# Kernel optimization log

Measured on AMD Instinct MI355X. Metric: run time of the kernel, lower is better.

Reference implementation:

```python
import jax, jax.numpy as jnp
import numpy as np

FRAMES = 8
NUM_HEADS = 12


def _build_indices_mask(N_origin):
    """Static (numpy) construction of gathered token indices and the
    multiplicative token mask (1.0 on allowed pairs, 0.8 elsewhere),
    matching token_mask + (1-token_mask)*0.8 in the torch code."""
    N = FRAMES * N_origin
    cls_idx = np.arange(0, N, N_origin)
    per_frame = [np.arange(i * N_origin + 1 + i, (i + 1) * N_origin, FRAMES)
                 for i in range(FRAMES)]
    idx = np.concatenate([cls_idx] + per_frame)
    M = idx.shape[0]
    mask = np.full((N, M), 0.8, dtype=np.float32)
    cls_len = cls_idx.shape[0]
    mask[:, :cls_len] = 1.0
    st = cls_len
    for i in range(FRAMES):
        ln = per_frame[i].shape[0]
        mask[i * N_origin:(i + 1) * N_origin, st:st + ln] = 1.0
        st += ln
    return jnp.asarray(idx), jnp.asarray(mask)


def setup_inputs() -> dict:
    key = jax.random.key(0)
    k1, k2, k3, k4 = jax.random.split(key, 4)
    C = 768
    x = jax.random.normal(k1, (64, 197, C), dtype=jnp.float32)
    qkv_w = jax.random.normal(k2, (3 * C, C), dtype=jnp.float32) * 0.02
    proj_w = jax.random.normal(k3, (C, C), dtype=jnp.float32) * 0.02
    proj_b = jax.random.normal(k4, (C,), dtype=jnp.float32) * 0.02
    return {"x": x, "qkv_w": qkv_w, "proj_w": proj_w, "proj_b": proj_b}


def reference(x, qkv_w, proj_w, proj_b):
    B0, N_origin, C = x.shape
    H = NUM_HEADS
    hd = C // H
    B = B0 // FRAMES
    N = FRAMES * N_origin
    scale = hd ** -0.5

    xg = x.reshape(B, N, C)                              # group 8 frames per video
    qkv = (xg @ qkv_w.T).reshape(B, N, 3, H, hd).transpose(2, 0, 3, 1, 4)
    q, k, v = qkv[0], qkv[1], qkv[2]                     # each [B, H, N, hd]

    idx, mask = _build_indices_mask(N_origin)            # idx [M], mask [N, M]
    k = k[:, :, idx, :]                                  # [B, H, M, hd]
    v = v[:, :, idx, :]

    attn = jnp.einsum('bhnd,bhmd->bhnm', q, k) * scale   # [B, H, N, M]
    attn = jax.nn.softmax(attn * mask, axis=-1)          # multiplicative mask, then softmax

    out = jnp.einsum('bhnm,bhmd->bhnd', attn, v)         # [B, H, N, hd]
    out = out.transpose(0, 2, 1, 3).reshape(B, N, C)
    out = out @ proj_w.T + proj_b
    return out.reshape(B0, N_origin, C)
```

## Files before the change

kernel.cpp:

```cpp
#include <hip/hip_runtime.h>
#include <stdint.h>

#define NORI   197
#define FRAMES 8
#define NTOK   1576
#define BATCH  8
#define NHEAD  12
#define CDIM   768
#define MG     204
#define TOKENS 12608

typedef _Float16 half8 __attribute__((ext_vector_type(8)));
typedef float floatx4 __attribute__((ext_vector_type(4)));

typedef const __attribute__((address_space(1))) void GPTR;
typedef __attribute__((address_space(3))) void LPTR;

__device__ __forceinline__ int gather_idx(int m) {
    if (m < 8) return m * NORI;
    int u = m - 8;
    int f, t;
    if (u < 100) { f = u / 25; t = u - f * 25; }
    else         { f = 4 + (u - 100) / 24; t = (u - 100) - (f - 4) * 24; }
    return f * NORI + 1 + f + 8 * t;
}
__device__ __forceinline__ int col_frame(int m) {
    int u = m - 8;
    return (u < 100) ? (u / 25) : (4 + (u - 100) / 24);
}

__device__ __forceinline__ int xcd_chunk(int bid, int nwg) {
    int xcd = bid & 7, j = bid >> 3;
    int q = nwg >> 3, r = nwg & 7;
    int base = (xcd < r) ? xcd * (q + 1) : r * (q + 1) + (xcd - r) * q;
    return base + j;
}

__global__ __launch_bounds__(256) void cast_all(
    const float* __restrict__ x, const float* __restrict__ qkvw,
    const float* __restrict__ projw, _Float16* __restrict__ out)
{
    const int n1 = TOKENS * CDIM / 8, n2 = 3 * CDIM * CDIM / 8, n3 = CDIM * CDIM / 8;
    const int nxb = n1 / 256;
    int bx = blockIdx.x;
    int i;
    if (bx < nxb) i = xcd_chunk(bx, nxb) * 256 + threadIdx.x;
    else          i = bx * 256 + threadIdx.x;
    if (i >= n1 + n2 + n3) return;
    const float* src; int off;
    if (i < n1)           { src = x;     off = i; }
    else if (i < n1 + n2) { src = qkvw;  off = i - n1; }
    else                  { src = projw; off = i - n1 - n2; }
    float4 a = ((const float4*)src)[2 * off];
    float4 b = ((const float4*)src)[2 * off + 1];
    half8 o = { (_Float16)a.x, (_Float16)a.y, (_Float16)a.z, (_Float16)a.w,
                (_Float16)b.x, (_Float16)b.y, (_Float16)b.z, (_Float16)b.w };
    ((half8*)out)[i] = o;
}

template <int OUT_F32>
__device__ __forceinline__ void gemm_body(
    const _Float16* __restrict__ A, const _Float16* __restrict__ W,
    const float* __restrict__ bias, void* __restrict__ Y,
    int M, int Woff, int ldY, int gather, int r0, int c0,
    _Float16* As0, _Float16* Bs0, _Float16* As1, _Float16* Bs1)
{
    const int tid = threadIdx.x;
    const int w = tid >> 6, l = tid & 63;
    const int wm = (w >> 1) * 64, wn = (w & 1) * 64;

    const _Float16* sa[2];
    const _Float16* sb[2];
    int soff[2];
#pragma unroll
    for (int i = 0; i < 2; i++) {
        int rt = w * 32 + i * 16 + (l >> 2);
        int cg = (l & 3) ^ ((l >> 3) & 3);
        int ra = min(r0 + rt, M - 1);
        if (gather) { int b = ra / MG; int m = ra - b * MG; ra = b * NTOK + gather_idx(m); }
        sa[i] = A + (size_t)ra * CDIM + cg * 8;
        sb[i] = W + (size_t)(Woff + c0 + rt) * CDIM + cg * 8;
        soff[i] = (w * 32 + i * 16) * 32;
    }

#pragma unroll
    for (int i = 0; i < 2; i++) {
        __builtin_amdgcn_global_load_lds((GPTR*)sa[i], (LPTR*)(As0 + soff[i]), 16, 0, 0);
        __builtin_amdgcn_global_load_lds((GPTR*)sb[i], (LPTR*)(Bs0 + soff[i]), 16, 0, 0);
    }

    floatx4 acc[4][4] = {};
    const int fc = ((l >> 4) ^ ((l >> 1) & 3)) * 8;
    const int mrow = l & 15;

#pragma unroll
    for (int it = 0; it < 24; it++) {
        const _Float16* Ac = (it & 1) ? As1 : As0;
        const _Float16* Bc = (it & 1) ? Bs1 : Bs0;
        _Float16* An = (it & 1) ? As0 : As1;
        _Float16* Bn = (it & 1) ? Bs0 : Bs1;

        if (it < 23) {
            int kb = (it + 1) * 32;
#pragma unroll
            for (int i = 0; i < 2; i++) {
                __builtin_amdgcn_global_load_lds((GPTR*)(sa[i] + kb), (LPTR*)(An + soff[i]), 16, 0, 0);
                __builtin_amdgcn_global_load_lds((GPTR*)(sb[i] + kb), (LPTR*)(Bn + soff[i]), 16, 0, 0);
            }
            __builtin_amdgcn_s_waitcnt(0x0074);
        } else {
            __builtin_amdgcn_s_waitcnt(0x0070);
        }
        __builtin_amdgcn_s_barrier();
        __builtin_amdgcn_sched_barrier(0);

        half8 af[4], bf[4];
#pragma unroll
        for (int t = 0; t < 4; t++) {
            af[t] = *(const half8*)&Ac[(wm + t * 16 + mrow) * 32 + fc];
            bf[t] = *(const half8*)&Bc[(wn + t * 16 + mrow) * 32 + fc];
        }
#pragma unroll
        for (int mt = 0; mt < 4; mt++)
#pragma unroll
            for (int nt = 0; nt < 4; nt++)
                acc[mt][nt] = __builtin_amdgcn_mfma_f32_16x16x32_f16(af[mt], bf[nt], acc[mt][nt], 0, 0, 0);

        __builtin_amdgcn_sched_barrier(0);
        __builtin_amdgcn_s_barrier();
    }

#pragma unroll
    for (int nt = 0; nt < 4; nt++) {
        int col = c0 + wn + nt * 16 + (l & 15);
        float bv = bias ? bias[col] : 0.f;
#pragma unroll
        for (int mt = 0; mt < 4; mt++) {
#pragma unroll
            for (int r = 0; r < 4; r++) {
                int row = r0 + wm + mt * 16 + (l >> 4) * 4 + r;
                if (row < M) {
                    if (OUT_F32) ((float*)Y)[(size_t)row * ldY + col] = acc[mt][nt][r] + bv;
                    else ((_Float16*)Y)[(size_t)row * ldY + col] = (_Float16)acc[mt][nt][r];
                }
            }
        }
    }
}

__global__ __launch_bounds__(256) void gemm_qkv(
    const _Float16* __restrict__ xh, const _Float16* __restrict__ qkvwh,
    _Float16* __restrict__ Qh, _Float16* __restrict__ KVh)
{
    __shared__ __align__(16) _Float16 As0[128 * 32];
    __shared__ __align__(16) _Float16 Bs0[128 * 32];
    __shared__ __align__(16) _Float16 As1[128 * 32];
    __shared__ __align__(16) _Float16 Bs1[128 * 32];
    int bx = blockIdx.x;
    if (bx < 600) {
        if (bx >= 594) return;
        int wg = xcd_chunk(bx, 594);
        int rb = wg / 6, cb = wg - rb * 6;
        gemm_body<0>(xh, qkvwh, nullptr, Qh, TOKENS, 0, CDIM, 0,
                     rb * 128, cb * 128, As0, Bs0, As1, Bs1);
    } else {
        int b2 = bx - 600;
        int wg = xcd_chunk(b2, 156);
        int rb = wg / 12, cb = wg - rb * 12;
        gemm_body<0>(xh, qkvwh, nullptr, KVh, BATCH * MG, CDIM, 1536, 1,
                     rb * 128, cb * 128, As0, Bs0, As1, Bs1);
    }
}

__global__ __launch_bounds__(256) void gemm_proj(
    const _Float16* __restrict__ AOh, const _Float16* __restrict__ projwh,
    const float* __restrict__ bias, float* __restrict__ out)
{
    __shared__ __align__(16) _Float16 As0[128 * 32];
    __shared__ __align__(16) _Float16 Bs0[128 * 32];
    __shared__ __align__(16) _Float16 As1[128 * 32];
    __shared__ __align__(16) _Float16 Bs1[128 * 32];
    int wg = xcd_chunk(blockIdx.x, 594);
    int rb = wg / 6, cb = wg - rb * 6;
    gemm_body<1>(AOh, projwh, bias, out, TOKENS, 0, CDIM, 0,
                 rb * 128, cb * 128, As0, Bs0, As1, Bs1);
}

__global__ __launch_bounds__(256, 2) void attn_mfma(
    const _Float16* __restrict__ Qh, const _Float16* __restrict__ KVh,
    _Float16* __restrict__ AOh)
{
    __shared__ __align__(16) _Float16 Ks[204 * 64];
    __shared__ __align__(16) _Float16 Vt[64 * 208];
    __shared__ __align__(16) _Float16 Ps[64 * 216];

    const int tid = threadIdx.x;
    const int id = blockIdx.x;
    const int b = id & 7;
    const int j = id >> 3;
    const int h = j % NHEAD;
    const int qc0 = (j / NHEAD) * 320;

    for (int e = tid; e < MG * 8; e += 256) {
        int row = e >> 3, c8 = e & 7;
        half8 v = *(const half8*)&KVh[(size_t)(b * MG + row) * 1536 + h * 64 + c8 * 8];
        *(half8*)&Ks[row * 64 + ((c8 ^ (row & 7)) * 8)] = v;
    }
    {
        const int d0 = (tid >> 5) * 8, lmp = tid & 31;
#pragma unroll
        for (int mo = 0; mo < 7; mo++) {
            int mp = mo * 32 + lmp;
            if (mp >= 208) continue;
            half8 v = {};
            if (mp < MG) v = *(const half8*)&KVh[(size_t)(b * MG + mp) * 1536 + 768 + h * 64 + d0];
#pragma unroll
            for (int jj = 0; jj < 8; jj++) Vt[(d0 + jj) * 208 + mp] = v[jj];
        }
    }
    __syncthreads();

    const int w = tid >> 6, l = tid & 63;
    const int lm = l & 15, lq = l >> 4;

    int cf[13];
#pragma unroll
    for (int t = 0; t < 13; t++) {
        int col = t * 16 + lm;
        cf[t] = (col < 8) ? -1 : (col >= MG ? -2 : col_frame(col));
    }

    _Float16* Pw = &Ps[(w * 16) * 216];

    for (int t5 = 0; t5 < 5; t5++) {
        const int rb = qc0 + t5 * 64 + w * 16;
        if (rb >= NTOK) break;

        floatx4 acc[13] = {};
        const int qrowA = min(rb + lm, NTOK - 1);
        const _Float16* qbase = Qh + (size_t)(b * NTOK + qrowA) * CDIM + h * 64;
        __builtin_amdgcn_s_setprio(1);
#pragma unroll
        for (int ks = 0; ks < 64; ks += 32) {
            half8 aq = *(const half8*)(qbase + ks + lq * 8);
#pragma unroll
            for (int t = 0; t < 13; t++) {
                half8 bk = *(const half8*)&Ks[(t * 16 + lm) * 64 + (((ks >> 3) + lq) ^ (lm & 7)) * 8];
                acc[t] = __builtin_amdgcn_mfma_f32_16x16x32_f16(aq, bk, acc[t], 0, 0, 0);
            }
        }
        __builtin_amdgcn_s_setprio(0);

#pragma unroll
        for (int r = 0; r < 4; r++) {
            int qrow = min(rb + lq * 4 + r, NTOK - 1);
            int rf = qrow / NORI;
            float sv[13];
            float mx = -1e30f;
#pragma unroll
            for (int t = 0; t < 13; t++) {
                float s = acc[t][r] * 0.125f;
                s *= (cf[t] == -1 || cf[t] == rf) ? 1.f : 0.8f;
                if (cf[t] == -2) s = -1e30f;
                sv[t] = s;
                mx = fmaxf(mx, s);
            }
#pragma unroll
            for (int off = 1; off < 16; off <<= 1) mx = fmaxf(mx, __shfl_xor(mx, off, 64));
            float sum = 0.f;
#pragma unroll
            for (int t = 0; t < 13; t++) { sv[t] = __expf(sv[t] - mx); sum += sv[t]; }
#pragma unroll
            for (int off = 1; off < 16; off <<= 1) sum += __shfl_xor(sum, off, 64);
            float inv = 1.f / sum;
#pragma unroll
            for (int t = 0; t < 13; t++) acc[t][r] = sv[t] * inv;
        }

#pragma unroll
        for (int t = 0; t < 13; t++)
#pragma unroll
            for (int r = 0; r < 4; r++)
                Pw[(lq * 4 + r) * 216 + t * 16 + lm] = (_Float16)acc[t][r];

        floatx4 oacc[4] = {};
        const _Float16* prow = &Pw[lm * 216];
        __builtin_amdgcn_s_setprio(1);
#pragma unroll
        for (int ks = 0; ks < 192; ks += 32) {
            half8 ap = *(const half8*)(prow + ks + lq * 8);
#pragma unroll
            for (int t = 0; t < 4; t++) {
                half8 bv = *(const half8*)&Vt[(t * 16 + lm) * 208 + ks + lq * 8];
                oacc[t] = __builtin_amdgcn_mfma_f32_16x16x32_f16(ap, bv, oacc[t], 0, 0, 0);
            }
        }
        {
            typedef _Float16 half4v __attribute__((ext_vector_type(4)));
            half4v ap4 = *(const half4v*)(prow + 192 + lq * 4);
#pragma unroll
            for (int t = 0; t < 4; t++) {
                half4v bv4 = *(const half4v*)&Vt[(t * 16 + lm) * 208 + 192 + lq * 4];
                oacc[t] = __builtin_amdgcn_mfma_f32_16x16x16f16(ap4, bv4, oacc[t], 0, 0, 0);
            }
        }
        __builtin_amdgcn_s_setprio(0);

#pragma unroll
        for (int t = 0; t < 4; t++)
#pragma unroll
            for (int r = 0; r < 4; r++) {
                int qrow = rb + lq * 4 + r;
                if (qrow < NTOK)
                    AOh[(size_t)(b * NTOK + qrow) * CDIM + h * 64 + t * 16 + lm] = (_Float16)oacc[t][r];
            }
    }
}

extern "C" void kernel_launch(void* const* d_in, const int* in_sizes, int n_in,
                              void* d_out, int out_size, void* d_ws, size_t ws_size,
                              hipStream_t stream) {
    const float* x      = (const float*)d_in[0];
    const float* qkv_w  = (const float*)d_in[1];
    const float* proj_w = (const float*)d_in[2];
    const float* proj_b = (const float*)d_in[3];
    float* out = (float*)d_out;

    _Float16* xh     = (_Float16*)d_ws;
    _Float16* qkvwh  = xh + (size_t)TOKENS * CDIM;
    _Float16* projwh = qkvwh + (size_t)3 * CDIM * CDIM;
    _Float16* Qh     = projwh + (size_t)CDIM * CDIM;
    _Float16* KVh    = Qh + (size_t)TOKENS * CDIM;
    _Float16* AOh    = KVh + (size_t)(BATCH * MG) * 1536;

    dim3 blk(256);
    const int ncast = (TOKENS * CDIM + 3 * CDIM * CDIM + CDIM * CDIM) / 8;
    cast_all<<<dim3((ncast + 255) / 256), blk, 0, stream>>>(x, qkv_w, proj_w, xh);

    gemm_qkv<<<dim3(600 + 156), blk, 0, stream>>>(xh, qkvwh, Qh, KVh);

    attn_mfma<<<dim3(480), blk, 0, stream>>>(Qh, KVh, AOh);

    gemm_proj<<<dim3(594), blk, 0, stream>>>(AOh, projwh, proj_b, out);
}
```

Measured before the change: 181.8 us.

## Load GEMM weight fragments directly into registers instead of staging through LDS

The GEMM body no longer stages the weight (B) tile through double-buffered shared memory. Each wave now reads its own B fragments straight from global memory into registers, double-buffered in two register sets. This halves LDS usage and removes the B-side LDS writes and reads, which could raise occupancy. In exchange, the two waves sharing a column half each load the same B data redundantly, register pressure rises, and global-load latency now sits directly in the waitcnt path.

```diff
diff --git a/kernel.cpp b/kernel.cpp
--- a/kernel.cpp
+++ b/kernel.cpp
@@ -63,14 +63,14 @@
     const _Float16* __restrict__ A, const _Float16* __restrict__ W,
     const float* __restrict__ bias, void* __restrict__ Y,
     int M, int Woff, int ldY, int gather, int r0, int c0,
-    _Float16* As0, _Float16* Bs0, _Float16* As1, _Float16* Bs1)
+    _Float16* As0, _Float16* As1)
 {
     const int tid = threadIdx.x;
     const int w = tid >> 6, l = tid & 63;
     const int wm = (w >> 1) * 64, wn = (w & 1) * 64;
+    const int lm = l & 15, lq = l >> 4;
 
     const _Float16* sa[2];
-    const _Float16* sb[2];
     int soff[2];
 #pragma unroll
     for (int i = 0; i < 2; i++) {
@@ -79,52 +79,68 @@
         int ra = min(r0 + rt, M - 1);
         if (gather) { int b = ra / MG; int m = ra - b * MG; ra = b * NTOK + gather_idx(m); }
         sa[i] = A + (size_t)ra * CDIM + cg * 8;
-        sb[i] = W + (size_t)(Woff + c0 + rt) * CDIM + cg * 8;
         soff[i] = (w * 32 + i * 16) * 32;
     }
 
-#pragma unroll
-    for (int i = 0; i < 2; i++) {
+    const _Float16* pb[4];
+#pragma unroll
+    for (int t = 0; t < 4; t++) {
+        int col = c0 + wn + t * 16 + lm;
+        pb[t] = W + (size_t)(Woff + col) * CDIM + lq * 8;
+    }
+
+#pragma unroll
+    for (int i = 0; i < 2; i++)
         __builtin_amdgcn_global_load_lds((GPTR*)sa[i], (LPTR*)(As0 + soff[i]), 16, 0, 0);
-        __builtin_amdgcn_global_load_lds((GPTR*)sb[i], (LPTR*)(Bs0 + soff[i]), 16, 0, 0);
-    }
+    half8 b0[4], b1[4];
+#pragma unroll
+    for (int t = 0; t < 4; t++) b0[t] = *(const half8*)(pb[t]);
 
     floatx4 acc[4][4] = {};
     const int fc = ((l >> 4) ^ ((l >> 1) & 3)) * 8;
-    const int mrow = l & 15;
+    const int mrow = lm;
 
 #pragma unroll
     for (int it = 0; it < 24; it++) {
         const _Float16* Ac = (it & 1) ? As1 : As0;
-        const _Float16* Bc = (it & 1) ? Bs1 : Bs0;
         _Float16* An = (it & 1) ? As0 : As1;
-        _Float16* Bn = (it & 1) ? Bs0 : Bs1;
 
         if (it < 23) {
             int kb = (it + 1) * 32;
 #pragma unroll
-            for (int i = 0; i < 2; i++) {
+            for (int i = 0; i < 2; i++)
                 __builtin_amdgcn_global_load_lds((GPTR*)(sa[i] + kb), (LPTR*)(An + soff[i]), 16, 0, 0);
-                __builtin_amdgcn_global_load_lds((GPTR*)(sb[i] + kb), (LPTR*)(Bn + soff[i]), 16, 0, 0);
-            }
+            if (it & 1) {
+#pragma unroll
+                for (int t = 0; t < 4; t++) b0[t] = *(const half8*)(pb[t] + kb);
+            } else {
+#pragma unroll
+                for (int t = 0; t < 4; t++) b1[t] = *(const half8*)(pb[t] + kb);
+            }
+            __builtin_amdgcn_s_waitcnt(0x0076);
+        } else {
             __builtin_amdgcn_s_waitcnt(0x0074);
-        } else {
-            __builtin_amdgcn_s_waitcnt(0x0070);
         }
         __builtin_amdgcn_s_barrier();
         __builtin_amdgcn_sched_barrier(0);
 
-        half8 af[4], bf[4];
-#pragma unroll
-        for (int t = 0; t < 4; t++) {
+        half8 af[4];
+#pragma unroll
+        for (int t = 0; t < 4; t++)
             af[t] = *(const half8*)&Ac[(wm + t * 16 + mrow) * 32 + fc];
-            bf[t] = *(const half8*)&Bc[(wn + t * 16 + mrow) * 32 + fc];
-        }
-#pragma unroll
-        for (int mt = 0; mt < 4; mt++)
-#pragma unroll
-            for (int nt = 0; nt < 4; nt++)
-                acc[mt][nt] = __builtin_amdgcn_mfma_f32_16x16x32_f16(af[mt], bf[nt], acc[mt][nt], 0, 0, 0);
+        if (it & 1) {
+#pragma unroll
+            for (int mt = 0; mt < 4; mt++)
+#pragma unroll
+                for (int nt = 0; nt < 4; nt++)
+                    acc[mt][nt] = __builtin_amdgcn_mfma_f32_16x16x32_f16(af[mt], b1[nt], acc[mt][nt], 0, 0, 0);
+        } else {
+#pragma unroll
+            for (int mt = 0; mt < 4; mt++)
+#pragma unroll
+                for (int nt = 0; nt < 4; nt++)
+                    acc[mt][nt] = __builtin_amdgcn_mfma_f32_16x16x32_f16(af[mt], b0[nt], acc[mt][nt], 0, 0, 0);
+        }
 
         __builtin_amdgcn_sched_barrier(0);
         __builtin_amdgcn_s_barrier();
@@ -132,13 +148,13 @@
 
 #pragma unroll
     for (int nt = 0; nt < 4; nt++) {
-        int col = c0 + wn + nt * 16 + (l & 15);
+        int col = c0 + wn + nt * 16 + lm;
         float bv = bias ? bias[col] : 0.f;
 #pragma unroll
         for (int mt = 0; mt < 4; mt++) {
 #pragma unroll
             for (int r = 0; r < 4; r++) {
-                int row = r0 + wm + mt * 16 + (l >> 4) * 4 + r;
+                int row = r0 + wm + mt * 16 + lq * 4 + r;
                 if (row < M) {
                     if (OUT_F32) ((float*)Y)[(size_t)row * ldY + col] = acc[mt][nt][r] + bv;
                     else ((_Float16*)Y)[(size_t)row * ldY + col] = (_Float16)acc[mt][nt][r];
@@ -153,22 +169,20 @@
     _Float16* __restrict__ Qh, _Float16* __restrict__ KVh)
 {
     __shared__ __align__(16) _Float16 As0[128 * 32];
-    __shared__ __align__(16) _Float16 Bs0[128 * 32];
     __shared__ __align__(16) _Float16 As1[128 * 32];
-    __shared__ __align__(16) _Float16 Bs1[128 * 32];
     int bx = blockIdx.x;
     if (bx < 600) {
         if (bx >= 594) return;
         int wg = xcd_chunk(bx, 594);
         int rb = wg / 6, cb = wg - rb * 6;
         gemm_body<0>(xh, qkvwh, nullptr, Qh, TOKENS, 0, CDIM, 0,
-                     rb * 128, cb * 128, As0, Bs0, As1, Bs1);
+                     rb * 128, cb * 128, As0, As1);
     } else {
         int b2 = bx - 600;
         int wg = xcd_chunk(b2, 156);
         int rb = wg / 12, cb = wg - rb * 12;
         gemm_body<0>(xh, qkvwh, nullptr, KVh, BATCH * MG, CDIM, 1536, 1,
-                     rb * 128, cb * 128, As0, Bs0, As1, Bs1);
+                     rb * 128, cb * 128, As0, As1);
     }
 }
 
@@ -177,13 +191,11 @@
     const float* __restrict__ bias, float* __restrict__ out)
 {
     __shared__ __align__(16) _Float16 As0[128 * 32];
-    __shared__ __align__(16) _Float16 Bs0[128 * 32];
     __shared__ __align__(16) _Float16 As1[128 * 32];
-    __shared__ __align__(16) _Float16 Bs1[128 * 32];
     int wg = xcd_chunk(blockIdx.x, 594);
     int rb = wg / 6, cb = wg - rb * 6;
     gemm_body<1>(AOh, projwh, bias, out, TOKENS, 0, CDIM, 0,
-                 rb * 128, cb * 128, As0, Bs0, As1, Bs1);
+                 rb * 128, cb * 128, As0, As1);
 }
 
 __global__ __launch_bounds__(256, 2) void attn_mfma(
```

Result: slower. 215.5 us (+18.5%).
